# Kernel tuning notes

Measured on AMD Instinct MI355X. Metric: run time of the kernel, lower is better.

Reference implementation:

```python
import jax, jax.numpy as jnp
import numpy as np

N_HEADS = 4
N_GROUPS = 32
EPS = 1e-5


def setup_inputs() -> dict:
    key = jax.random.key(0)
    ks = jax.random.split(key, 6)
    c = 512
    x = jax.random.normal(ks[0], (4, c, 64, 64), dtype=jnp.float32)
    # conv1x1 weights ~ kaiming-ish scale
    s = 1.0 / np.sqrt(c)
    wq = jax.random.normal(ks[1], (c, c), dtype=jnp.float32) * s
    wk = jax.random.normal(ks[2], (c, c), dtype=jnp.float32) * s
    wv = jax.random.normal(ks[3], (c, c), dtype=jnp.float32) * s
    wp = jax.random.normal(ks[4], (c, c), dtype=jnp.float32) * s
    zeros = jnp.zeros((c,), dtype=jnp.float32)
    return {
        "x": x,
        "gn_w": jnp.ones((c,), dtype=jnp.float32), "gn_b": zeros,
        "wq": wq, "bq": zeros, "wk": wk, "bk": zeros,
        "wv": wv, "bv": zeros, "wp": wp, "bp": zeros,
    }


def _group_norm(x, w, b):
    bsz, c, h, wd = x.shape
    xg = x.reshape(bsz, N_GROUPS, c // N_GROUPS, h, wd)
    mean = xg.mean(axis=(2, 3, 4), keepdims=True)
    var = xg.var(axis=(2, 3, 4), keepdims=True)
    xg = (xg - mean) * jax.lax.rsqrt(var + EPS)
    x = xg.reshape(bsz, c, h, wd)
    return x * w[None, :, None, None] + b[None, :, None, None]


def _conv1x1(x, w, b):
    # x: (b,c,h,w), w: (out,in) -> (b,out,h,w)
    return jnp.einsum('bchw,oc->bohw', x, w) + b[None, :, None, None]


def reference(x, gn_w, gn_b, wq, bq, wk, bk, wv, bv, wp, bp):
    bsz, c, h, wd = x.shape
    hd = c // N_HEADS
    hw = h * wd
    x_n = _group_norm(x, gn_w, gn_b)
    q = _conv1x1(x_n, wq, bq)
    k = _conv1x1(x_n, wk, bk)
    v = _conv1x1(x_n, wv, bv)

    def to_heads(t):
        # (b,c,h,w) -> (b, n_heads, hw, head_dim)
        return t.reshape(bsz, N_HEADS, hd, hw).transpose(0, 1, 3, 2)

    q, k, v = to_heads(q), to_heads(k), to_heads(v)
    scale = hd ** (-0.5)
    attn = jnp.einsum('bhqd,bhkd->bhqk', q, k) * scale  # (b,H,hw,hw)
    attn = jax.nn.softmax(attn, axis=-1)
    out = jnp.einsum('bhqk,bhkd->bhqd', attn, v)
    out = out.transpose(0, 1, 3, 2).reshape(bsz, c, h, wd)
    out = _conv1x1(out, wp, bp)
    return x + out
```

## Files before the change

kernel.cpp:

```cpp
#include <hip/hip_runtime.h>
#include <math.h>

typedef __attribute__((ext_vector_type(8))) short short8;
typedef __attribute__((ext_vector_type(4))) float floatx4;
typedef __attribute__((ext_vector_type(16))) float floatx16;
typedef __attribute__((ext_vector_type(8))) unsigned short ushort8v;
typedef __attribute__((ext_vector_type(4))) unsigned short ushort4v;

#define HW 4096
#define CCH 512
#define NB 4
#define NH 4
#define HD 128

__device__ __forceinline__ unsigned short f2bf(float f) {
    union { float f; unsigned int u; } c; c.f = f;
    unsigned int u = c.u;
    u += 0x7FFFu + ((u >> 16) & 1u);
    return (unsigned short)(u >> 16);
}

__global__ void conv_w(const float* __restrict__ w0, const float* __restrict__ w1,
                       const float* __restrict__ w2, const float* __restrict__ w3,
                       unsigned short* __restrict__ dst) {
    const float* src = blockIdx.y == 0 ? w0 : blockIdx.y == 1 ? w1 : blockIdx.y == 2 ? w2 : w3;
    unsigned short* d = dst + (size_t)blockIdx.y * 262144;
    int i = blockIdx.x * 256 + threadIdx.x;
    float4 v = ((const float4*)src)[i];
    ushort4v o;
    o[0] = f2bf(v.x); o[1] = f2bf(v.y); o[2] = f2bf(v.z); o[3] = f2bf(v.w);
    ((ushort4v*)d)[i] = o;
}

__global__ void gn_stats(const float* __restrict__ x, float* __restrict__ stats) {
    int bg = blockIdx.x;
    int b = bg >> 5, g = bg & 31;
    const float4* p = (const float4*)(x + ((size_t)b * CCH + g * 16) * HW);
    float s = 0.f, ss = 0.f;
    for (int i = threadIdx.x; i < 16384; i += 256) {
        float4 v = p[i];
        s  += v.x + v.y + v.z + v.w;
        ss += v.x * v.x + v.y * v.y + v.z * v.z + v.w * v.w;
    }
    #pragma unroll
    for (int off = 32; off > 0; off >>= 1) {
        s  += __shfl_down(s, off, 64);
        ss += __shfl_down(ss, off, 64);
    }
    __shared__ float sm[4], sm2[4];
    int wid = threadIdx.x >> 6;
    if ((threadIdx.x & 63) == 0) { sm[wid] = s; sm2[wid] = ss; }
    __syncthreads();
    if (threadIdx.x == 0) {
        float ts = sm[0] + sm[1] + sm[2] + sm[3];
        float tss = sm2[0] + sm2[1] + sm2[2] + sm2[3];
        float mean = ts * (1.f / 65536.f);
        float var = tss * (1.f / 65536.f) - mean * mean;
        stats[bg * 2] = mean;
        stats[bg * 2 + 1] = rsqrtf(var + 1e-5f);
    }
}

__global__ void gn_apply(const float* __restrict__ x, const float* __restrict__ gnw,
                         const float* __restrict__ gnb, const float* __restrict__ stats,
                         unsigned short* __restrict__ xt) {
    int s = blockIdx.x * 256 + threadIdx.x;
    int g = blockIdx.y, b = blockIdx.z;
    float mean = stats[(b * 32 + g) * 2];
    float rstd = stats[(b * 32 + g) * 2 + 1];
    const float* xb = x + ((size_t)b * CCH + g * 16) * HW + s;
    unsigned short outv[16];
    #pragma unroll
    for (int cl = 0; cl < 16; cl++) {
        int c = g * 16 + cl;
        float v = xb[(size_t)cl * HW];
        v = (v - mean) * rstd * gnw[c] + gnb[c];
        outv[cl] = f2bf(v);
    }
    unsigned short* dst = xt + ((size_t)b * HW + s) * CCH + g * 16;
    *(ushort8v*)dst       = *(ushort8v*)&outv[0];
    *(ushort8v*)(dst + 8) = *(ushort8v*)&outv[8];
}

#define LDP 72
template <int MODE>
__global__ __launch_bounds__(256, 2) void gemm_nt(
    const unsigned short* __restrict__ A, long long aStride,
    const unsigned short* __restrict__ Bm, long long bStride,
    const float* __restrict__ bias, float scale,
    const float* __restrict__ resid, long long rStride,
    void* __restrict__ Cp, long long cStride, int ldc) {
    __shared__ unsigned short lA[2][128 * LDP];
    __shared__ unsigned short lB[2][128 * LDP];
    const int tid = threadIdx.x;
    const int lane = tid & 63;
    const int wid = tid >> 6;
    const int z = blockIdx.z;
    const unsigned short* Ab = A + (size_t)z * aStride + (size_t)blockIdx.x * 128 * 512;
    const unsigned short* Bb = Bm + (size_t)z * bStride + (size_t)blockIdx.y * 128 * 512;

    floatx4 acc[4][4];
    #pragma unroll
    for (int i = 0; i < 4; i++)
        #pragma unroll
        for (int j = 0; j < 4; j++) acc[i][j] = (floatx4)0.f;

    const int wm = (wid >> 1) * 64;
    const int wn = (wid & 1) * 64;
    const int l15 = lane & 15;
    const int l4 = lane >> 4;
    const int srow = tid >> 3;
    const int skc  = (tid & 7) * 8;

    ushort8v ar[4], br[4];
    #pragma unroll
    for (int i = 0; i < 4; i++) {
        int row = srow + i * 32;
        ar[i] = *(const ushort8v*)&Ab[(size_t)row * 512 + skc];
        br[i] = *(const ushort8v*)&Bb[(size_t)row * 512 + skc];
    }
    #pragma unroll
    for (int i = 0; i < 4; i++) {
        int row = srow + i * 32;
        *(ushort8v*)&lA[0][row * LDP + skc] = ar[i];
        *(ushort8v*)&lB[0][row * LDP + skc] = br[i];
    }
    __syncthreads();

    int cur = 0;
    #pragma unroll 1
    for (int t = 0; t < 8; t++) {
        if (t < 7) {
            int k0 = (t + 1) * 64;
            #pragma unroll
            for (int i = 0; i < 4; i++) {
                int row = srow + i * 32;
                ar[i] = *(const ushort8v*)&Ab[(size_t)row * 512 + k0 + skc];
                br[i] = *(const ushort8v*)&Bb[(size_t)row * 512 + k0 + skc];
            }
        }
        #pragma unroll
        for (int kk = 0; kk < 2; kk++) {
            short8 af[4], bf[4];
            #pragma unroll
            for (int i = 0; i < 4; i++)
                af[i] = *(const short8*)&lA[cur][(wm + i * 16 + l15) * LDP + kk * 32 + l4 * 8];
            #pragma unroll
            for (int j = 0; j < 4; j++)
                bf[j] = *(const short8*)&lB[cur][(wn + j * 16 + l15) * LDP + kk * 32 + l4 * 8];
            #pragma unroll
            for (int i = 0; i < 4; i++)
                #pragma unroll
                for (int j = 0; j < 4; j++)
                    acc[i][j] = __builtin_amdgcn_mfma_f32_16x16x32_bf16(af[i], bf[j], acc[i][j], 0, 0, 0);
        }
        if (t < 7) {
            int nxt = cur ^ 1;
            #pragma unroll
            for (int i = 0; i < 4; i++) {
                int row = srow + i * 32;
                *(ushort8v*)&lA[nxt][row * LDP + skc] = ar[i];
                *(ushort8v*)&lB[nxt][row * LDP + skc] = br[i];
            }
            __syncthreads();
            cur = nxt;
        }
    }

    long long m0 = (long long)blockIdx.x * 128 + wm;
    long long n0 = (long long)blockIdx.y * 128 + wn;
    if (MODE == 0 || MODE == 3) {
        unsigned short* C = (unsigned short*)Cp + (size_t)z * cStride;
        const float* bptr = (MODE == 3 && z == 1) ? resid : bias;
        float sc = (MODE == 3 && z == 1) ? 1.f : scale;
        #pragma unroll
        for (int i = 0; i < 4; i++)
            #pragma unroll
            for (int j = 0; j < 4; j++) {
                long long col = n0 + j * 16 + l15;
                float bv = bptr[col];
                #pragma unroll
                for (int r = 0; r < 4; r++) {
                    long long row = m0 + i * 16 + l4 * 4 + r;
                    C[row * ldc + col] = f2bf((acc[i][j][r] + bv) * sc);
                }
            }
    } else if (MODE == 1) {
        float* C = (float*)Cp + (size_t)z * cStride;
        const float* R = resid + (size_t)z * rStride;
        #pragma unroll
        for (int i = 0; i < 4; i++)
            #pragma unroll
            for (int j = 0; j < 4; j++)
                #pragma unroll
                for (int r = 0; r < 4; r++) {
                    long long row = m0 + i * 16 + l4 * 4 + r;
                    long long col = n0 + j * 16 + l15;
                    C[row * ldc + col] = acc[i][j][r] + bias[row] + R[row * ldc + col];
                }
    } else {
        unsigned short* C = (unsigned short*)Cp + (size_t)z * cStride;
        #pragma unroll
        for (int i = 0; i < 4; i++)
            #pragma unroll
            for (int j = 0; j < 4; j++)
                #pragma unroll
                for (int r = 0; r < 4; r++) {
                    long long row = m0 + i * 16 + l4 * 4 + r;
                    long long col = n0 + j * 16 + l15;
                    C[row * ldc + col] = f2bf(acc[i][j][r] + bias[row]);
                }
    }
}

#define LQP 136
#define LTP 72
__global__ __launch_bounds__(256, 2) void attn_kern(
    const unsigned short* __restrict__ Qb, const unsigned short* __restrict__ Kb,
    const unsigned short* __restrict__ Vt, unsigned short* __restrict__ Ob) {
    __shared__ unsigned short lk[2][64 * LQP];
    __shared__ unsigned short lvt[2][128 * LTP];
    const int tid = threadIdx.x;
    const int lane = tid & 63;
    const int w = tid >> 6;
    const int l31 = lane & 31;
    const int l1 = lane >> 5;
    const int q0 = blockIdx.x * 128;
    const int h = blockIdx.y, b = blockIdx.z;
    const size_t headOff = (size_t)h * HD;
    const size_t batchRow = (size_t)b * HW;
    const unsigned short* VtB = Vt + ((size_t)b * CCH + headOff) * HW;

    short8 qf[8];
    #pragma unroll
    for (int kd = 0; kd < 8; kd++)
        qf[kd] = *(const short8*)&Qb[(batchRow + q0 + w * 32 + l31) * 512
                                     + headOff + kd * 16 + l1 * 8];

    short8 onesf;
    #pragma unroll
    for (int e = 0; e < 8; e++) onesf[e] = (short)0x3F80;

    floatx16 acc_o[4];
    floatx16 acc_l;
    acc_l = (floatx16)0.f;
    #pragma unroll
    for (int dj = 0; dj < 4; dj++) acc_o[dj] = (floatx16)0.f;

    ushort8v kreg[4], vreg[4];
    #pragma unroll
    for (int i = 0; i < 4; i++) {
        int idx = i * 256 + tid;
        kreg[i] = *(const ushort8v*)&Kb[(batchRow + (idx >> 4)) * 512 + headOff + (idx & 15) * 8];
        vreg[i] = *(const ushort8v*)&VtB[(size_t)(idx >> 3) * HW + (idx & 7) * 8];
    }
    #pragma unroll
    for (int i = 0; i < 4; i++) {
        int idx = i * 256 + tid;
        *(ushort8v*)&lk[0][(idx >> 4) * LQP + (idx & 15) * 8] = kreg[i];
        *(ushort8v*)&lvt[0][(idx >> 3) * LTP + (idx & 7) * 8] = vreg[i];
    }
    __syncthreads();

    int cur = 0;
    for (int kt = 0; kt < 64; kt++) {
        const unsigned short* lkc  = lk[cur];
        const unsigned short* lvtc = lvt[cur];

        if (kt < 63) {
            int t0n = (kt + 1) * 64;
            #pragma unroll
            for (int i = 0; i < 4; i++) {
                int idx = i * 256 + tid;
                kreg[i] = *(const ushort8v*)&Kb[(batchRow + t0n + (idx >> 4)) * 512 + headOff + (idx & 15) * 8];
                vreg[i] = *(const ushort8v*)&VtB[(size_t)(idx >> 3) * HW + t0n + (idx & 7) * 8];
            }
        }

        floatx16 sa0 = (floatx16)0.f;
        floatx16 sa1 = (floatx16)0.f;
        __builtin_amdgcn_s_setprio(1);
        #pragma unroll
        for (int kd = 0; kd < 8; kd++) {
            short8 kf0 = *(const short8*)&lkc[(l31) * LQP + kd * 16 + l1 * 8];
            short8 kf1 = *(const short8*)&lkc[(32 + l31) * LQP + kd * 16 + l1 * 8];
            sa0 = __builtin_amdgcn_mfma_f32_32x32x16_bf16(kf0, qf[kd], sa0, 0, 0, 0);
            sa1 = __builtin_amdgcn_mfma_f32_32x32x16_bf16(kf1, qf[kd], sa1, 0, 0, 0);
        }
        __builtin_amdgcn_s_setprio(0);

        short8 paf0, paf1;
        {
            #pragma unroll
            for (int r = 0; r < 16; r++) sa0[r] = __builtin_amdgcn_exp2f(sa0[r]);
            unsigned int wv[4][2];
            #pragma unroll
            for (int g = 0; g < 4; g++) {
                asm("v_cvt_pk_bf16_f32 %0, %1, %2" : "=v"(wv[g][0])
                    : "v"(sa0[4 * g + 0]), "v"(sa0[4 * g + 1]));
                asm("v_cvt_pk_bf16_f32 %0, %1, %2" : "=v"(wv[g][1])
                    : "v"(sa0[4 * g + 2]), "v"(sa0[4 * g + 3]));
            }
            unsigned int a0 = wv[0][0], b0 = wv[1][0], a1 = wv[0][1], b1 = wv[1][1];
            asm("v_permlane32_swap_b32 %0, %1" : "+v"(a0), "+v"(b0));
            asm("v_permlane32_swap_b32 %0, %1" : "+v"(a1), "+v"(b1));
            union { unsigned int u[4]; short8 s8; } f0;
            f0.u[0] = a0; f0.u[1] = a1; f0.u[2] = b0; f0.u[3] = b1;
            paf0 = f0.s8;
            unsigned int c0 = wv[2][0], d0 = wv[3][0], c1 = wv[2][1], d1 = wv[3][1];
            asm("v_permlane32_swap_b32 %0, %1" : "+v"(c0), "+v"(d0));
            asm("v_permlane32_swap_b32 %0, %1" : "+v"(c1), "+v"(d1));
            union { unsigned int u[4]; short8 s8; } f1;
            f1.u[0] = c0; f1.u[1] = c1; f1.u[2] = d0; f1.u[3] = d1;
            paf1 = f1.s8;
        }

        __builtin_amdgcn_s_setprio(1);
        acc_l = __builtin_amdgcn_mfma_f32_32x32x16_bf16(paf0, onesf, acc_l, 0, 0, 0);
        #pragma unroll
        for (int dj = 0; dj < 4; dj++) {
            short8 vv = *(const short8*)&lvtc[(dj * 32 + l31) * LTP + 0 * 16 + l1 * 8];
            acc_o[dj] = __builtin_amdgcn_mfma_f32_32x32x16_bf16(paf0, vv, acc_o[dj], 0, 0, 0);
        }
        acc_l = __builtin_amdgcn_mfma_f32_32x32x16_bf16(paf1, onesf, acc_l, 0, 0, 0);
        #pragma unroll
        for (int dj = 0; dj < 4; dj++) {
            short8 vv = *(const short8*)&lvtc[(dj * 32 + l31) * LTP + 1 * 16 + l1 * 8];
            acc_o[dj] = __builtin_amdgcn_mfma_f32_32x32x16_bf16(paf1, vv, acc_o[dj], 0, 0, 0);
        }
        __builtin_amdgcn_s_setprio(0);

        short8 paf2, paf3;
        {
            #pragma unroll
            for (int r = 0; r < 16; r++) sa1[r] = __builtin_amdgcn_exp2f(sa1[r]);
            unsigned int wv[4][2];
            #pragma unroll
            for (int g = 0; g < 4; g++) {
                asm("v_cvt_pk_bf16_f32 %0, %1, %2" : "=v"(wv[g][0])
                    : "v"(sa1[4 * g + 0]), "v"(sa1[4 * g + 1]));
                asm("v_cvt_pk_bf16_f32 %0, %1, %2" : "=v"(wv[g][1])
                    : "v"(sa1[4 * g + 2]), "v"(sa1[4 * g + 3]));
            }
            unsigned int a0 = wv[0][0], b0 = wv[1][0], a1 = wv[0][1], b1 = wv[1][1];
            asm("v_permlane32_swap_b32 %0, %1" : "+v"(a0), "+v"(b0));
            asm("v_permlane32_swap_b32 %0, %1" : "+v"(a1), "+v"(b1));
            union { unsigned int u[4]; short8 s8; } f2;
            f2.u[0] = a0; f2.u[1] = a1; f2.u[2] = b0; f2.u[3] = b1;
            paf2 = f2.s8;
            unsigned int c0 = wv[2][0], d0 = wv[3][0], c1 = wv[2][1], d1 = wv[3][1];
            asm("v_permlane32_swap_b32 %0, %1" : "+v"(c0), "+v"(d0));
            asm("v_permlane32_swap_b32 %0, %1" : "+v"(c1), "+v"(d1));
            union { unsigned int u[4]; short8 s8; } f3;
            f3.u[0] = c0; f3.u[1] = c1; f3.u[2] = d0; f3.u[3] = d1;
            paf3 = f3.s8;
        }

        __builtin_amdgcn_s_setprio(1);
        acc_l = __builtin_amdgcn_mfma_f32_32x32x16_bf16(paf2, onesf, acc_l, 0, 0, 0);
        #pragma unroll
        for (int dj = 0; dj < 4; dj++) {
            short8 vv = *(const short8*)&lvtc[(dj * 32 + l31) * LTP + 2 * 16 + l1 * 8];
            acc_o[dj] = __builtin_amdgcn_mfma_f32_32x32x16_bf16(paf2, vv, acc_o[dj], 0, 0, 0);
        }
        acc_l = __builtin_amdgcn_mfma_f32_32x32x16_bf16(paf3, onesf, acc_l, 0, 0, 0);
        #pragma unroll
        for (int dj = 0; dj < 4; dj++) {
            short8 vv = *(const short8*)&lvtc[(dj * 32 + l31) * LTP + 3 * 16 + l1 * 8];
            acc_o[dj] = __builtin_amdgcn_mfma_f32_32x32x16_bf16(paf3, vv, acc_o[dj], 0, 0, 0);
        }
        __builtin_amdgcn_s_setprio(0);

        if (kt < 63) {
            int nxt = cur ^ 1;
            #pragma unroll
            for (int i = 0; i < 4; i++) {
                int idx = i * 256 + tid;
                *(ushort8v*)&lk[nxt][(idx >> 4) * LQP + (idx & 15) * 8] = kreg[i];
                *(ushort8v*)&lvt[nxt][(idx >> 3) * LTP + (idx & 7) * 8] = vreg[i];
            }
            __syncthreads();
            cur = nxt;
        }
    }

    #pragma unroll
    for (int g = 0; g < 4; g++)
        #pragma unroll
        for (int p = 0; p < 4; p++) {
            int reg = 4 * g + p;
            float rl = 1.f / acc_l[reg];
            int qr = p + 8 * g + 4 * l1;
            size_t row = batchRow + q0 + w * 32 + qr;
            #pragma unroll
            for (int dj = 0; dj < 4; dj++)
                Ob[row * 512 + headOff + dj * 32 + l31] = f2bf(acc_o[dj][reg] * rl);
        }
}

extern "C" void kernel_launch(void* const* d_in, const int* in_sizes, int n_in,
                              void* d_out, int out_size, void* d_ws, size_t ws_size,
                              hipStream_t stream) {
    const float* x   = (const float*)d_in[0];
    const float* gnw = (const float*)d_in[1];
    const float* gnb = (const float*)d_in[2];
    const float* wq  = (const float*)d_in[3];
    const float* bq  = (const float*)d_in[4];
    const float* wk  = (const float*)d_in[5];
    const float* bk  = (const float*)d_in[6];
    const float* wv  = (const float*)d_in[7];
    const float* bv  = (const float*)d_in[8];
    const float* wp  = (const float*)d_in[9];
    const float* bp  = (const float*)d_in[10];
    float* out = (float*)d_out;

    const size_t NE = (size_t)NB * HW * CCH;
    unsigned short* ws16 = (unsigned short*)d_ws;
    unsigned short* XT = ws16;
    unsigned short* Qb = ws16 + NE;
    unsigned short* Kb = ws16 + 2 * NE;
    unsigned short* Vt = ws16 + 3 * NE;
    unsigned short* Wb = ws16 + 4 * NE;
    float* stats = (float*)(ws16 + 4 * NE + 4 * 262144);

    const float qscale = 0.08838834764831845f * 1.4426950408889634f;

    conv_w<<<dim3(256, 4), 256, 0, stream>>>(wq, wk, wv, wp, Wb);
    gn_stats<<<128, 256, 0, stream>>>(x, stats);
    gn_apply<<<dim3(16, 32, 4), 256, 0, stream>>>(x, gnw, gnb, stats, XT);

    gemm_nt<3><<<dim3(128, 4, 2), 256, 0, stream>>>(XT, 0, Wb, 262144, bq, qscale, bk, 0,
                                                    Qb, (long long)NE, 512);
    gemm_nt<2><<<dim3(4, 32, 4), 256, 0, stream>>>(Wb + 2 * 262144, 0, XT, (long long)HW * 512, bv, 1.f,
                                                   nullptr, 0, Vt, (long long)CCH * HW, HW);

    unsigned short* Ob = XT;
    attn_kern<<<dim3(32, NH, NB), 256, 0, stream>>>(Qb, Kb, Vt, Ob);

    gemm_nt<1><<<dim3(4, 32, 4), 256, 0, stream>>>(Wb + 3 * 262144, 0, Ob, (long long)HW * 512, bp, 1.f,
                                                   x, (long long)CCH * HW, out, (long long)CCH * HW, HW);
}
```

Baseline: 346.8 us.

## Use direct global-to-LDS loads with XOR swizzle and software-pipeline QK across iterations

Replaces the register-staged K/V tile loads with global_load_lds direct-to-LDS transfers. The padded shared layout becomes an XOR-swizzled unpadded one to avoid bank conflicts. The attention loop is software-pipelined so that the QK^T MFMAs for tile kt+1 are interleaved with the PV MFMAs for tile kt, and K is prefetched two tiles ahead. The aim is to cut VGPR pressure and LDS store instructions and to raise MFMA overlap with the exp work, at the cost of more LDS buffers and a more complex schedule.

```diff
diff --git a/kernel.cpp b/kernel.cpp
--- a/kernel.cpp
+++ b/kernel.cpp
@@ -18,6 +18,12 @@
     unsigned int u = c.u;
     u += 0x7FFFu + ((u >> 16) & 1u);
     return (unsigned short)(u >> 16);
+}
+
+__device__ __forceinline__ void gload_lds16(const unsigned short* g, unsigned short* l) {
+    __builtin_amdgcn_global_load_lds(
+        (const __attribute__((address_space(1))) unsigned int*)g,
+        (__attribute__((address_space(3))) unsigned int*)l, 16, 0, 0);
 }
 
 __global__ void conv_w(const float* __restrict__ w0, const float* __restrict__ w1,
@@ -213,13 +219,11 @@
     }
 }
 
-#define LQP 136
-#define LTP 72
 __global__ __launch_bounds__(256, 2) void attn_kern(
     const unsigned short* __restrict__ Qb, const unsigned short* __restrict__ Kb,
     const unsigned short* __restrict__ Vt, unsigned short* __restrict__ Ob) {
-    __shared__ unsigned short lk[2][64 * LQP];
-    __shared__ unsigned short lvt[2][128 * LTP];
+    __shared__ __align__(16) unsigned short lk0[8192], lk1[8192];
+    __shared__ __align__(16) unsigned short lv0[8192], lv1[8192];
     const int tid = threadIdx.x;
     const int lane = tid & 63;
     const int w = tid >> 6;
@@ -231,6 +235,22 @@
     const size_t batchRow = (size_t)b * HW;
     const unsigned short* VtB = Vt + ((size_t)b * CCH + headOff) * HW;
 
+    size_t kSrc[4], vSrc[4];
+    #pragma unroll
+    for (int n = 0; n < 4; n++) {
+        int row = w * 16 + n * 4 + (lane >> 4);
+        int sk = ((row & 7) << 1) | ((row >> 3) & 1);
+        int jk = (lane & 15) ^ sk;
+        kSrc[n] = (batchRow + row) * 512 + headOff + jk * 8;
+        int d = w * 32 + n * 8 + (lane >> 3);
+        int jv = (lane & 7) ^ (d & 7);
+        vSrc[n] = (size_t)d * HW + jv * 8;
+    }
+    const int ldsOff = w * 4 * 512;
+
+    const int sk0 = ((l31 & 7) << 1) | ((l31 >> 3) & 1);
+    const int sv0 = l31 & 7;
+
     short8 qf[8];
     #pragma unroll
     for (int kd = 0; kd < 8; kd++)
@@ -247,141 +267,136 @@
     #pragma unroll
     for (int dj = 0; dj < 4; dj++) acc_o[dj] = (floatx16)0.f;
 
-    ushort8v kreg[4], vreg[4];
-    #pragma unroll
-    for (int i = 0; i < 4; i++) {
-        int idx = i * 256 + tid;
-        kreg[i] = *(const ushort8v*)&Kb[(batchRow + (idx >> 4)) * 512 + headOff + (idx & 15) * 8];
-        vreg[i] = *(const ushort8v*)&VtB[(size_t)(idx >> 3) * HW + (idx & 7) * 8];
-    }
-    #pragma unroll
-    for (int i = 0; i < 4; i++) {
-        int idx = i * 256 + tid;
-        *(ushort8v*)&lk[0][(idx >> 4) * LQP + (idx & 15) * 8] = kreg[i];
-        *(ushort8v*)&lvt[0][(idx >> 3) * LTP + (idx & 7) * 8] = vreg[i];
-    }
+    #pragma unroll
+    for (int n = 0; n < 4; n++) gload_lds16(&Kb[kSrc[n]], lk0 + ldsOff + n * 512);
+    #pragma unroll
+    for (int n = 0; n < 4; n++) gload_lds16(&Kb[kSrc[n] + (size_t)64 * 512], lk1 + ldsOff + n * 512);
+    #pragma unroll
+    for (int n = 0; n < 4; n++) gload_lds16(&VtB[vSrc[n]], lv0 + ldsOff + n * 512);
     __syncthreads();
 
-    int cur = 0;
-    for (int kt = 0; kt < 64; kt++) {
-        const unsigned short* lkc  = lk[cur];
-        const unsigned short* lvtc = lvt[cur];
-
-        if (kt < 63) {
-            int t0n = (kt + 1) * 64;
-            #pragma unroll
-            for (int i = 0; i < 4; i++) {
-                int idx = i * 256 + tid;
-                kreg[i] = *(const ushort8v*)&Kb[(batchRow + t0n + (idx >> 4)) * 512 + headOff + (idx & 15) * 8];
-                vreg[i] = *(const ushort8v*)&VtB[(size_t)(idx >> 3) * HW + t0n + (idx & 7) * 8];
-            }
-        }
-
-        floatx16 sa0 = (floatx16)0.f;
-        floatx16 sa1 = (floatx16)0.f;
-        __builtin_amdgcn_s_setprio(1);
-        #pragma unroll
-        for (int kd = 0; kd < 8; kd++) {
-            short8 kf0 = *(const short8*)&lkc[(l31) * LQP + kd * 16 + l1 * 8];
-            short8 kf1 = *(const short8*)&lkc[(32 + l31) * LQP + kd * 16 + l1 * 8];
-            sa0 = __builtin_amdgcn_mfma_f32_32x32x16_bf16(kf0, qf[kd], sa0, 0, 0, 0);
-            sa1 = __builtin_amdgcn_mfma_f32_32x32x16_bf16(kf1, qf[kd], sa1, 0, 0, 0);
-        }
-        __builtin_amdgcn_s_setprio(0);
-
-        short8 paf0, paf1;
+    floatx16 sa0 = (floatx16)0.f, sa1 = (floatx16)0.f;
+    #pragma unroll
+    for (int kd = 0; kd < 8; kd++) {
+        int xk = ((kd * 2 + l1) ^ sk0) * 8;
+        short8 kf0 = *(const short8*)&lk0[l31 * 128 + xk];
+        short8 kf1 = *(const short8*)&lk0[l31 * 128 + xk + 4096];
+        sa0 = __builtin_amdgcn_mfma_f32_32x32x16_bf16(kf0, qf[kd], sa0, 0, 0, 0);
+        sa1 = __builtin_amdgcn_mfma_f32_32x32x16_bf16(kf1, qf[kd], sa1, 0, 0, 0);
+    }
+    __syncthreads();
+
+    unsigned short* lvCur = lv0;  unsigned short* lvNxt = lv1;
+    unsigned short* kRead = lk1;  unsigned short* kWrite = lk0;
+
+    #pragma unroll 1
+    for (int kt = 0; kt < 63; kt++) {
         {
-            #pragma unroll
-            for (int r = 0; r < 16; r++) sa0[r] = __builtin_amdgcn_exp2f(sa0[r]);
+            size_t tv = (size_t)(kt + 1) * 64;
+            size_t tk = (size_t)(kt + 2) * 64 * 512;
+            #pragma unroll
+            for (int n = 0; n < 4; n++) gload_lds16(&VtB[vSrc[n] + tv], lvNxt + ldsOff + n * 512);
+            #pragma unroll
+            for (int n = 0; n < 4; n++) gload_lds16(&Kb[kSrc[n] + tk], kWrite + ldsOff + n * 512);
+        }
+
+        short8 paf[4];
+        #pragma unroll
+        for (int r = 0; r < 16; r++) sa0[r] = __builtin_amdgcn_exp2f(sa0[r]);
+        #pragma unroll
+        for (int r = 0; r < 16; r++) sa1[r] = __builtin_amdgcn_exp2f(sa1[r]);
+        #pragma unroll
+        for (int tb = 0; tb < 2; tb++) {
+            const floatx16& sa = tb ? sa1 : sa0;
             unsigned int wv[4][2];
             #pragma unroll
             for (int g = 0; g < 4; g++) {
                 asm("v_cvt_pk_bf16_f32 %0, %1, %2" : "=v"(wv[g][0])
-                    : "v"(sa0[4 * g + 0]), "v"(sa0[4 * g + 1]));
+                    : "v"(sa[4 * g + 0]), "v"(sa[4 * g + 1]));
                 asm("v_cvt_pk_bf16_f32 %0, %1, %2" : "=v"(wv[g][1])
-                    : "v"(sa0[4 * g + 2]), "v"(sa0[4 * g + 3]));
-            }
-            unsigned int a0 = wv[0][0], b0 = wv[1][0], a1 = wv[0][1], b1 = wv[1][1];
-            asm("v_permlane32_swap_b32 %0, %1" : "+v"(a0), "+v"(b0));
-            asm("v_permlane32_swap_b32 %0, %1" : "+v"(a1), "+v"(b1));
-            union { unsigned int u[4]; short8 s8; } f0;
-            f0.u[0] = a0; f0.u[1] = a1; f0.u[2] = b0; f0.u[3] = b1;
-            paf0 = f0.s8;
-            unsigned int c0 = wv[2][0], d0 = wv[3][0], c1 = wv[2][1], d1 = wv[3][1];
-            asm("v_permlane32_swap_b32 %0, %1" : "+v"(c0), "+v"(d0));
-            asm("v_permlane32_swap_b32 %0, %1" : "+v"(c1), "+v"(d1));
-            union { unsigned int u[4]; short8 s8; } f1;
-            f1.u[0] = c0; f1.u[1] = c1; f1.u[2] = d0; f1.u[3] = d1;
-            paf1 = f1.s8;
-        }
-
+                    : "v"(sa[4 * g + 2]), "v"(sa[4 * g + 3]));
+            }
+            #pragma unroll
+            for (int hh = 0; hh < 2; hh++) {
+                unsigned int a0 = wv[2 * hh][0], b0 = wv[2 * hh + 1][0];
+                unsigned int a1 = wv[2 * hh][1], b1 = wv[2 * hh + 1][1];
+                asm("v_permlane32_swap_b32 %0, %1" : "+v"(a0), "+v"(b0));
+                asm("v_permlane32_swap_b32 %0, %1" : "+v"(a1), "+v"(b1));
+                union { unsigned int u[4]; short8 s8; } f;
+                f.u[0] = a0; f.u[1] = a1; f.u[2] = b0; f.u[3] = b1;
+                paf[2 * tb + hh] = f.s8;
+            }
+        }
+
+        sa0 = (floatx16)0.f; sa1 = (floatx16)0.f;
         __builtin_amdgcn_s_setprio(1);
-        acc_l = __builtin_amdgcn_mfma_f32_32x32x16_bf16(paf0, onesf, acc_l, 0, 0, 0);
-        #pragma unroll
-        for (int dj = 0; dj < 4; dj++) {
-            short8 vv = *(const short8*)&lvtc[(dj * 32 + l31) * LTP + 0 * 16 + l1 * 8];
-            acc_o[dj] = __builtin_amdgcn_mfma_f32_32x32x16_bf16(paf0, vv, acc_o[dj], 0, 0, 0);
-        }
-        acc_l = __builtin_amdgcn_mfma_f32_32x32x16_bf16(paf1, onesf, acc_l, 0, 0, 0);
-        #pragma unroll
-        for (int dj = 0; dj < 4; dj++) {
-            short8 vv = *(const short8*)&lvtc[(dj * 32 + l31) * LTP + 1 * 16 + l1 * 8];
-            acc_o[dj] = __builtin_amdgcn_mfma_f32_32x32x16_bf16(paf1, vv, acc_o[dj], 0, 0, 0);
+        #pragma unroll
+        for (int u = 0; u < 4; u++) {
+            #pragma unroll
+            for (int q2 = 0; q2 < 2; q2++) {
+                int kd = u * 2 + q2;
+                int xk = ((kd * 2 + l1) ^ sk0) * 8;
+                short8 kf0 = *(const short8*)&kRead[l31 * 128 + xk];
+                short8 kf1 = *(const short8*)&kRead[l31 * 128 + xk + 4096];
+                sa0 = __builtin_amdgcn_mfma_f32_32x32x16_bf16(kf0, qf[kd], sa0, 0, 0, 0);
+                sa1 = __builtin_amdgcn_mfma_f32_32x32x16_bf16(kf1, qf[kd], sa1, 0, 0, 0);
+            }
+            acc_l = __builtin_amdgcn_mfma_f32_32x32x16_bf16(paf[u], onesf, acc_l, 0, 0, 0);
+            int xv = ((u * 2 + l1) ^ sv0) * 8;
+            #pragma unroll
+            for (int dj = 0; dj < 4; dj++) {
+                short8 vv = *(const short8*)&lvCur[dj * 2048 + l31 * 64 + xv];
+                acc_o[dj] = __builtin_amdgcn_mfma_f32_32x32x16_bf16(paf[u], vv, acc_o[dj], 0, 0, 0);
+            }
         }
         __builtin_amdgcn_s_setprio(0);
 
-        short8 paf2, paf3;
-        {
-            #pragma unroll
-            for (int r = 0; r < 16; r++) sa1[r] = __builtin_amdgcn_exp2f(sa1[r]);
+        __syncthreads();
+        unsigned short* t;
+        t = lvCur; lvCur = lvNxt; lvNxt = t;
+        t = kRead; kRead = kWrite; kWrite = t;
+    }
+
+    {
+        short8 paf[4];
+        #pragma unroll
+        for (int r = 0; r < 16; r++) sa0[r] = __builtin_amdgcn_exp2f(sa0[r]);
+        #pragma unroll
+        for (int r = 0; r < 16; r++) sa1[r] = __builtin_amdgcn_exp2f(sa1[r]);
+        #pragma unroll
+        for (int tb = 0; tb < 2; tb++) {
+            const floatx16& sa = tb ? sa1 : sa0;
             unsigned int wv[4][2];
             #pragma unroll
             for (int g = 0; g < 4; g++) {
                 asm("v_cvt_pk_bf16_f32 %0, %1, %2" : "=v"(wv[g][0])
-                    : "v"(sa1[4 * g + 0]), "v"(sa1[4 * g + 1]));
+                    : "v"(sa[4 * g + 0]), "v"(sa[4 * g + 1]));
                 asm("v_cvt_pk_bf16_f32 %0, %1, %2" : "=v"(wv[g][1])
-                    : "v"(sa1[4 * g + 2]), "v"(sa1[4 * g + 3]));
-            }
-            unsigned int a0 = wv[0][0], b0 = wv[1][0], a1 = wv[0][1], b1 = wv[1][1];
-            asm("v_permlane32_swap_b32 %0, %1" : "+v"(a0), "+v"(b0));
-            asm("v_permlane32_swap_b32 %0, %1" : "+v"(a1), "+v"(b1));
-            union { unsigned int u[4]; short8 s8; } f2;
-            f2.u[0] = a0; f2.u[1] = a1; f2.u[2] = b0; f2.u[3] = b1;
-            paf2 = f2.s8;
-            unsigned int c0 = wv[2][0], d0 = wv[3][0], c1 = wv[2][1], d1 = wv[3][1];
-            asm("v_permlane32_swap_b32 %0, %1" : "+v"(c0), "+v"(d0));
-            asm("v_permlane32_swap_b32 %0, %1" : "+v"(c1), "+v"(d1));
-            union { unsigned int u[4]; short8 s8; } f3;
-            f3.u[0] = c0; f3.u[1] = c1; f3.u[2] = d0; f3.u[3] = d1;
-            paf3 = f3.s8;
-        }
-
+                    : "v"(sa[4 * g + 2]), "v"(sa[4 * g + 3]));
+            }
+            #pragma unroll
+            for (int hh = 0; hh < 2; hh++) {
+                unsigned int a0 = wv[2 * hh][0], b0 = wv[2 * hh + 1][0];
+                unsigned int a1 = wv[2 * hh][1], b1 = wv[2 * hh + 1][1];
+                asm("v_permlane32_swap_b32 %0, %1" : "+v"(a0), "+v"(b0));
+                asm("v_permlane32_swap_b32 %0, %1" : "+v"(a1), "+v"(b1));
+                union { unsigned int u[4]; short8 s8; } f;
+                f.u[0] = a0; f.u[1] = a1; f.u[2] = b0; f.u[3] = b1;
+                paf[2 * tb + hh] = f.s8;
+            }
+        }
         __builtin_amdgcn_s_setprio(1);
-        acc_l = __builtin_amdgcn_mfma_f32_32x32x16_bf16(paf2, onesf, acc_l, 0, 0, 0);
-        #pragma unroll
-        for (int dj = 0; dj < 4; dj++) {
-            short8 vv = *(const short8*)&lvtc[(dj * 32 + l31) * LTP + 2 * 16 + l1 * 8];
-            acc_o[dj] = __builtin_amdgcn_mfma_f32_32x32x16_bf16(paf2, vv, acc_o[dj], 0, 0, 0);
-        }
-        acc_l = __builtin_amdgcn_mfma_f32_32x32x16_bf16(paf3, onesf, acc_l, 0, 0, 0);
-        #pragma unroll
-        for (int dj = 0; dj < 4; dj++) {
-            short8 vv = *(const short8*)&lvtc[(dj * 32 + l31) * LTP + 3 * 16 + l1 * 8];
-            acc_o[dj] = __builtin_amdgcn_mfma_f32_32x32x16_bf16(paf3, vv, acc_o[dj], 0, 0, 0);
+        #pragma unroll
+        for (int u = 0; u < 4; u++) {
+            acc_l = __builtin_amdgcn_mfma_f32_32x32x16_bf16(paf[u], onesf, acc_l, 0, 0, 0);
+            int xv = ((u * 2 + l1) ^ sv0) * 8;
+            #pragma unroll
+            for (int dj = 0; dj < 4; dj++) {
+                short8 vv = *(const short8*)&lvCur[dj * 2048 + l31 * 64 + xv];
+                acc_o[dj] = __builtin_amdgcn_mfma_f32_32x32x16_bf16(paf[u], vv, acc_o[dj], 0, 0, 0);
+            }
         }
         __builtin_amdgcn_s_setprio(0);
-
-        if (kt < 63) {
-            int nxt = cur ^ 1;
-            #pragma unroll
-            for (int i = 0; i < 4; i++) {
-                int idx = i * 256 + tid;
-                *(ushort8v*)&lk[nxt][(idx >> 4) * LQP + (idx & 15) * 8] = kreg[i];
-                *(ushort8v*)&lvt[nxt][(idx >> 3) * LTP + (idx & 7) * 8] = vreg[i];
-            }
-            __syncthreads();
-            cur = nxt;
-        }
     }
 
     #pragma unroll
```

New measurement: 332.8 us. 1.04x faster.
